# Kernel tuning notes

Hardware: AMD Instinct MI355X
Metric: run time of the kernel (lower is better)

The kernel has to match this reference:

```python
import jax, jax.numpy as jnp
import numpy as np

N_NODES = 50000
N_EDGES = 800000
FEAT = 128
HID1 = 128
HID2 = 64


def setup_inputs() -> dict:
    key = jax.random.key(0)
    k = jax.random.split(key, 6)
    x = jax.random.normal(k[0], (N_NODES, FEAT), dtype=jnp.float32)
    edge_index = jax.random.randint(k[1], (2, N_EDGES), 0, N_NODES, dtype=jnp.int32)
    # Glorot-style init scaling like PyG's GCNConv linear
    W1 = jax.random.normal(k[2], (FEAT, HID1), dtype=jnp.float32) * (1.0 / np.sqrt(FEAT))
    b1 = jnp.zeros((HID1,), dtype=jnp.float32)
    W2 = jax.random.normal(k[3], (HID1, HID2), dtype=jnp.float32) * (1.0 / np.sqrt(HID1))
    b2 = jnp.zeros((HID2,), dtype=jnp.float32)
    return {"x": x, "edge_index": edge_index, "W1": W1, "b1": b1, "W2": W2, "b2": b2}


def _gcn_conv(x, src, dst, W, b, n_nodes):
    """PyG GCNConv: h = X W; out_i = sum_j norm_ij h_j + b, with self-loops and
    symmetric normalization norm_ij = deg_i^-1/2 * deg_j^-1/2 (deg counts self-loop)."""
    h = x @ W  # [N, out]
    # degree at target nodes (self-loops already appended to src/dst)
    deg = jax.ops.segment_sum(jnp.ones_like(dst, dtype=h.dtype), dst, num_segments=n_nodes)
    dinv = jax.lax.rsqrt(jnp.maximum(deg, 1.0))  # deg >= 1 because of self-loops
    norm = dinv[src] * dinv[dst]  # [E+N]
    msg = h[src] * norm[:, None]  # gather + scale, [E+N, out]
    out = jax.ops.segment_sum(msg, dst, num_segments=n_nodes)
    return out + b


def reference(x, edge_index, W1, b1, W2, b2):
    n = x.shape[0]
    self_idx = jnp.arange(n, dtype=edge_index.dtype)
    src = jnp.concatenate([edge_index[0], self_idx])
    dst = jnp.concatenate([edge_index[1], self_idx])
    h = jax.nn.relu(_gcn_conv(x, src, dst, W1, b1, n))
    out = _gcn_conv(h, src, dst, W2, b2, n)
    return out
```

## Files before the change

kernel.cpp:

```cpp
#include <hip/hip_runtime.h>
#include <hip/hip_bf16.h>


#define POISON 0xAAAAAAAAu

typedef __attribute__((ext_vector_type(8))) short short8;
typedef __attribute__((ext_vector_type(4))) float f32x4;

__device__ __forceinline__ float bf_lo(unsigned u) { return __uint_as_float(u << 16); }
__device__ __forceinline__ float bf_hi(unsigned u) { return __uint_as_float(u & 0xffff0000u); }
__device__ __forceinline__ unsigned short f2bf(float f) {
    return (unsigned short)(__bfloat16_as_ushort(__float2bfloat16(f)));
}

__global__ __launch_bounds__(256) void countpack_kernel(
    const int* __restrict__ dst, unsigned* __restrict__ ucnt,
    unsigned short* __restrict__ eslot, int E,
    const float* __restrict__ W1, unsigned short* __restrict__ Wp1,
    const float* __restrict__ W2, unsigned short* __restrict__ Wp2) {
    constexpr int PB = (128 * 128 + 128 * 64) / 256;
    if ((int)blockIdx.x < PB) {
        int q = blockIdx.x * 256 + threadIdx.x;
        if (q < 128 * 128) {
            int j = q & 7;
            int n = (q >> 3) & 127;
            int kb = q >> 10;
            Wp1[q] = f2bf(W1[(kb * 8 + j) * 128 + n]);
        } else {
            int p = q - 128 * 128;
            int j = p & 7;
            int n = (p >> 3) & 63;
            int kb = p >> 9;
            Wp2[p] = f2bf(W2[(kb * 8 + j) * 64 + n]);
        }
        return;
    }
    int e0 = (blockIdx.x - PB) * 1024 + threadIdx.x * 4;
    if (e0 + 3 < E) {
        int4 d4 = *(const int4*)(dst + e0);
        ushort4 r;
        r.x = (unsigned short)(atomicAdd(&ucnt[d4.x], 1u) - POISON);
        r.y = (unsigned short)(atomicAdd(&ucnt[d4.y], 1u) - POISON);
        r.z = (unsigned short)(atomicAdd(&ucnt[d4.z], 1u) - POISON);
        r.w = (unsigned short)(atomicAdd(&ucnt[d4.w], 1u) - POISON);
        *(ushort4*)(eslot + e0) = r;
    } else {
        for (int e = e0; e < E; ++e)
            eslot[e] = (unsigned short)(atomicAdd(&ucnt[dst[e]], 1u) - POISON);
    }
}

__global__ __launch_bounds__(256) void alloc_kernel(unsigned* __restrict__ ucnt,
                                                    int* __restrict__ row_ptr,
                                                    float* __restrict__ dinv, int N) {
    int i = blockIdx.x * 256 + threadIdx.x;
    int lane = threadIdx.x & 63;
    int c = (i < N) ? (int)(ucnt[i] - POISON) : 0;
    if (i < N) dinv[i] = rsqrtf((float)(c + 1));
    int incl = c;
#pragma unroll
    for (int off = 1; off < 64; off <<= 1) {
        int u = __shfl_up(incl, off, 64);
        if (lane >= off) incl += u;
    }
    int base = 0;
    if (lane == 63) base = (int)(atomicAdd(&ucnt[N], (unsigned)incl) - POISON);
    base = __shfl(base, 63, 64);
    if (i < N) row_ptr[i] = base + incl - c;
}

__global__ __launch_bounds__(256) void scatgemm_kernel(
    const int* __restrict__ src, const int* __restrict__ dst,
    const int* __restrict__ row_ptr, const unsigned short* __restrict__ eslot,
    unsigned short* __restrict__ ssrc, int E,
    const float* __restrict__ X, const unsigned short* __restrict__ Wp1,
    const float* __restrict__ dinv, unsigned short* __restrict__ g1,
    int N, int gb) {
    if ((int)blockIdx.x >= gb) {
        int e0 = (blockIdx.x - gb) * 1024 + threadIdx.x * 4;
        if (e0 + 3 < E) {
            int4 d4 = *(const int4*)(dst + e0);
            int4 s4 = *(const int4*)(src + e0);
            ushort4 t4 = *(const ushort4*)(eslot + e0);
            ssrc[row_ptr[d4.x] + t4.x] = (unsigned short)s4.x;
            ssrc[row_ptr[d4.y] + t4.y] = (unsigned short)s4.y;
            ssrc[row_ptr[d4.z] + t4.z] = (unsigned short)s4.z;
            ssrc[row_ptr[d4.w] + t4.w] = (unsigned short)s4.w;
        } else {
            for (int e = e0; e < E; ++e)
                ssrc[row_ptr[dst[e]] + eslot[e]] = (unsigned short)src[e];
        }
        return;
    }
    constexpr int NT = 8;
    const int lane = threadIdx.x & 63;
    const int wave = threadIdx.x >> 6;
    const int col = lane & 15;
    const int quad = lane >> 4;
    const int row0w = (blockIdx.x * 4 + wave) * 16;

    int arow = row0w + col;
    if (arow >= N) arow = N - 1;

    short8 afr[4];
    const float* Xr = X + (size_t)arow * 128;
#pragma unroll
    for (int c = 0; c < 4; ++c) {
        float4 f0 = *(const float4*)(Xr + c * 32 + quad * 8);
        float4 f1 = *(const float4*)(Xr + c * 32 + quad * 8 + 4);
        short8 a;
        a[0] = (short)f2bf(f0.x); a[1] = (short)f2bf(f0.y);
        a[2] = (short)f2bf(f0.z); a[3] = (short)f2bf(f0.w);
        a[4] = (short)f2bf(f1.x); a[5] = (short)f2bf(f1.y);
        a[6] = (short)f2bf(f1.z); a[7] = (short)f2bf(f1.w);
        afr[c] = a;
    }

    f32x4 acc[NT];
#pragma unroll
    for (int t = 0; t < NT; ++t) acc[t] = (f32x4){0.f, 0.f, 0.f, 0.f};

    const uint4* Wq = (const uint4*)Wp1;
#pragma unroll
    for (int c = 0; c < 4; ++c) {
        short8 bfr[NT];
#pragma unroll
        for (int t = 0; t < NT; ++t) {
            union { uint4 u; short8 s; } cv;
            cv.u = Wq[(size_t)(c * 4 + quad) * 128 + t * 16 + col];
            bfr[t] = cv.s;
        }
#pragma unroll
        for (int t = 0; t < NT; ++t)
            acc[t] = __builtin_amdgcn_mfma_f32_16x16x32_bf16(afr[c], bfr[t], acc[t], 0, 0, 0);
    }

#pragma unroll
    for (int r = 0; r < 4; ++r) {
        int row = row0w + quad * 4 + r;
        if (row < N) {
            float dv = dinv[row];
#pragma unroll
            for (int t = 0; t < NT; ++t)
                g1[(size_t)row * 128 + t * 16 + col] = f2bf(acc[t][r] * dv);
        }
    }
}

#define AG1_BURST(NS)                                            \
    do {                                                         \
        unsigned v[NS];                                          \
        _Pragma("unroll") for (int t = 0; t < NS; ++t) {         \
            int s = __shfl(sidx, t, 64);                         \
            if (t >= rem) s = node;                              \
            v[t] = hp[(size_t)s * 64 + lane];                    \
        }                                                        \
        _Pragma("unroll") for (int t = 0; t < NS; ++t) {         \
            unsigned u = (t < rem) ? v[t] : 0u;                  \
            ax += bf_lo(u);                                      \
            ay += bf_hi(u);                                      \
        }                                                        \
    } while (0)

__global__ __launch_bounds__(256) void aggmm_kernel(const unsigned short* __restrict__ g1,
                                                    const int* __restrict__ row_ptr,
                                                    const unsigned* __restrict__ ucnt,
                                                    const unsigned short* __restrict__ ssrc,
                                                    const float* __restrict__ dinv,
                                                    const float* __restrict__ b1,
                                                    const unsigned short* __restrict__ Wp2,
                                                    unsigned short* __restrict__ g2, int N) {
    __shared__ unsigned short zt[16][136];
    __shared__ float sdinv[16];
    const int lane = threadIdx.x & 63;
    const int wave = threadIdx.x >> 6;
    const int nodebase = blockIdx.x * 16;
    const unsigned* hp = (const unsigned*)g1;

    const float bx = b1[2 * lane];
    const float by = b1[2 * lane + 1];

    for (int k = 0; k < 4; ++k) {
        int zr = wave * 4 + k;
        int node = __builtin_amdgcn_readfirstlane(nodebase + zr);
        unsigned pk = 0;
        if (node < N) {
            float di = dinv[node];
            int beg = row_ptr[node];
            int cnt = (int)(ucnt[node] - POISON);
            unsigned hv = hp[(size_t)node * 64 + lane];
            float ax = bf_lo(hv), ay = bf_hi(hv);
            for (int ch = 0; ch < cnt; ch += 24) {
                int rem = cnt - ch;
                int sidx = (int)ssrc[beg + ch + (lane & 31)];
                if (rem <= 8) AG1_BURST(8);
                else if (rem <= 16) AG1_BURST(16);
                else AG1_BURST(24);
            }
            float zx = fmaxf(ax * di + bx, 0.f);
            float zy = fmaxf(ay * di + by, 0.f);
            pk = (unsigned)f2bf(zx) | ((unsigned)f2bf(zy) << 16);
            if (lane == 0) sdinv[zr] = di;
        } else if (lane == 0) {
            sdinv[zr] = 0.f;
        }
        ((unsigned*)&zt[zr][0])[lane] = pk;
    }
    __syncthreads();

    const int col = lane & 15;
    const int quad = lane >> 4;
    short8 afr[4];
#pragma unroll
    for (int c = 0; c < 4; ++c) {
        union { uint4 u; short8 s; } cv;
        cv.u = *(const uint4*)&zt[col][c * 32 + quad * 8];
        afr[c] = cv.s;
    }
    f32x4 acc = (f32x4){0.f, 0.f, 0.f, 0.f};
    const uint4* Wq = (const uint4*)Wp2;
#pragma unroll
    for (int c = 0; c < 4; ++c) {
        union { uint4 u; short8 s; } cv;
        cv.u = Wq[(size_t)(c * 4 + quad) * 64 + wave * 16 + col];
        acc = __builtin_amdgcn_mfma_f32_16x16x32_bf16(afr[c], cv.s, acc, 0, 0, 0);
    }
#pragma unroll
    for (int r = 0; r < 4; ++r) {
        int row = nodebase + quad * 4 + r;
        if (row < N)
            g2[(size_t)row * 64 + wave * 16 + col] = f2bf(acc[r] * sdinv[quad * 4 + r]);
    }
}

#define AG2_BURST(NS)                                            \
    do {                                                         \
        unsigned v[NS];                                          \
        _Pragma("unroll") for (int t = 0; t < NS; ++t) {         \
            int s = __shfl(sidx, t, 64);                         \
            if (t >= rem) s = node;                              \
            v[t] = (unsigned)gp[(size_t)s * 64 + lane];          \
        }                                                        \
        _Pragma("unroll") for (int t = 0; t < NS; ++t) {         \
            unsigned u = (t < rem) ? v[t] : 0u;                  \
            ax += bf_lo(u);                                      \
        }                                                        \
    } while (0)

__global__ __launch_bounds__(256) void agg2_kernel(const unsigned short* __restrict__ gp,
                                                   const int* __restrict__ row_ptr,
                                                   const unsigned* __restrict__ ucnt,
                                                   const unsigned short* __restrict__ ssrc,
                                                   const float* __restrict__ dinv,
                                                   const float* __restrict__ bias,
                                                   float* __restrict__ out, int N) {
    int node = __builtin_amdgcn_readfirstlane((int)(blockIdx.x * 4 + (threadIdx.x >> 6)));
    if (node >= N) return;
    int lane = threadIdx.x & 63;
    float di = dinv[node];
    int beg = row_ptr[node];
    int cnt = (int)(ucnt[node] - POISON);

    float ax = bf_lo((unsigned)gp[(size_t)node * 64 + lane]);
    for (int ch = 0; ch < cnt; ch += 24) {
        int rem = cnt - ch;
        int sidx = (int)ssrc[beg + ch + (lane & 31)];
        if (rem <= 8) AG2_BURST(8);
        else if (rem <= 16) AG2_BURST(16);
        else AG2_BURST(24);
    }
    out[(size_t)node * 64 + lane] = ax * di + bias[lane];
}

extern "C" void kernel_launch(void* const* d_in, const int* in_sizes, int n_in,
                              void* d_out, int out_size, void* d_ws, size_t ws_size,
                              hipStream_t stream) {
    const float* x = (const float*)d_in[0];
    const int* eidx = (const int*)d_in[1];
    const float* W1 = (const float*)d_in[2];
    const float* b1 = (const float*)d_in[3];
    const float* W2 = (const float*)d_in[4];
    const float* b2 = (const float*)d_in[5];
    float* out = (float*)d_out;

    const int N = in_sizes[0] / 128;
    const int E = in_sizes[1] / 2;
    const int* src = eidx;
    const int* dst = eidx + E;

    char* ws = (char*)d_ws;
    size_t off = 0;
    auto alloc = [&](size_t bytes) -> char* {
        char* p = ws + off;
        off = (off + bytes + 255) & ~(size_t)255;
        return p;
    };
    unsigned* ucnt = (unsigned*)alloc((size_t)(N + 1) * 4);
    int* row_ptr = (int*)alloc((size_t)N * 4);
    unsigned short* eslot = (unsigned short*)alloc((size_t)(E + 16) * 2);
    unsigned short* ssrc = (unsigned short*)alloc((size_t)(E + 64) * 2);
    float* dinv = (float*)alloc((size_t)N * 4);
    unsigned short* Wp1 = (unsigned short*)alloc(128 * 128 * 2);
    unsigned short* Wp2 = (unsigned short*)alloc(128 * 64 * 2);
    unsigned short* g1 = (unsigned short*)alloc((size_t)N * 128 * 2);
    unsigned short* g2 = (unsigned short*)alloc((size_t)N * 64 * 2);
    (void)alloc(9 << 20);

    const int nbN = (N + 255) / 256;
    const int nbE4 = (E + 1023) / 1024;
    const int gb = (N + 63) / 64;
    constexpr int PB = (128 * 128 + 128 * 64) / 256;

    countpack_kernel<<<PB + nbE4, 256, 0, stream>>>(dst, ucnt, eslot, E, W1, Wp1, W2, Wp2);
    alloc_kernel<<<nbN, 256, 0, stream>>>(ucnt, row_ptr, dinv, N);
    scatgemm_kernel<<<gb + nbE4, 256, 0, stream>>>(src, dst, row_ptr, eslot, ssrc, E,
                                                   x, Wp1, dinv, g1, N, gb);
    aggmm_kernel<<<(N + 15) / 16, 256, 0, stream>>>(g1, row_ptr, ucnt, ssrc, dinv, b1, Wp2, g2, N);
    agg2_kernel<<<(N + 3) / 4, 256, 0, stream>>>(g2, row_ptr, ucnt, ssrc, dinv, b2, out, N);
}
```

Measured before the change: 192.9 us.

## Fuse five GCN kernels into one cooperative persistent kernel with grid syncs

Replaces the chain of five kernel launches (count/pack, allocate, scatter+GEMM, aggregate+GEMM, aggregate) with a single cooperative persistent kernel. The stages run in grid-stride loops separated by grid.sync(). The goal is to remove launch overhead and the inter-kernel drain gaps. In exchange, occupancy is capped at the cooperative grid size and each stage runs with fewer blocks. Grid-wide barriers add their own cost, and the original kernels remain as a fallback if the cooperative launch fails.

```diff
diff --git a/kernel.cpp b/kernel.cpp
--- a/kernel.cpp
+++ b/kernel.cpp
@@ -1,5 +1,8 @@
 #include <hip/hip_runtime.h>
 #include <hip/hip_bf16.h>
+#include <hip/hip_cooperative_groups.h>
+
+namespace cg = cooperative_groups;
 
 
 #define POISON 0xAAAAAAAAu
@@ -11,6 +14,262 @@
 __device__ __forceinline__ float bf_hi(unsigned u) { return __uint_as_float(u & 0xffff0000u); }
 __device__ __forceinline__ unsigned short f2bf(float f) {
     return (unsigned short)(__bfloat16_as_ushort(__float2bfloat16(f)));
+}
+
+#define AG1_BURST(NS)                                            \
+    do {                                                         \
+        unsigned v[NS];                                          \
+        _Pragma("unroll") for (int t = 0; t < NS; ++t) {         \
+            int s = __shfl(sidx, t, 64);                         \
+            if (t >= rem) s = node;                              \
+            v[t] = hp[(size_t)s * 64 + lane];                    \
+        }                                                        \
+        _Pragma("unroll") for (int t = 0; t < NS; ++t) {         \
+            unsigned u = (t < rem) ? v[t] : 0u;                  \
+            ax += bf_lo(u);                                      \
+            ay += bf_hi(u);                                      \
+        }                                                        \
+    } while (0)
+
+#define AG2_BURST(NS)                                            \
+    do {                                                         \
+        unsigned v[NS];                                          \
+        _Pragma("unroll") for (int t = 0; t < NS; ++t) {         \
+            int s = __shfl(sidx, t, 64);                         \
+            if (t >= rem) s = node;                              \
+            v[t] = (unsigned)gp[(size_t)s * 64 + lane];          \
+        }                                                        \
+        _Pragma("unroll") for (int t = 0; t < NS; ++t) {         \
+            unsigned u = (t < rem) ? v[t] : 0u;                  \
+            ax += bf_lo(u);                                      \
+        }                                                        \
+    } while (0)
+
+struct GcnParams {
+    const int* src;
+    const int* dst;
+    unsigned* ucnt;
+    int* row_ptr;
+    unsigned short* eslot;
+    unsigned short* ssrc;
+    float* dinv;
+    const float* X;
+    const float* W1;
+    const float* b1;
+    const float* W2;
+    const float* b2;
+    unsigned short* Wp1;
+    unsigned short* Wp2;
+    unsigned short* g1;
+    unsigned short* g2;
+    float* out;
+    int N, E, gb, nbN, nbE4, ngrp16, ngrp4;
+};
+
+__global__ __launch_bounds__(256, 6) void gcn_mega(GcnParams p) {
+    cg::grid_group grid = cg::this_grid();
+    const int tid = threadIdx.x;
+    const int lane = tid & 63;
+    const int wave = tid >> 6;
+    const int nblk = (int)gridDim.x;
+
+    __shared__ unsigned short zt[16][136];
+    __shared__ float sdinv[16];
+
+    for (int q = blockIdx.x * 256 + tid; q < 128 * 128 + 128 * 64; q += nblk * 256) {
+        if (q < 128 * 128) {
+            int j = q & 7;
+            int n = (q >> 3) & 127;
+            int kb = q >> 10;
+            p.Wp1[q] = f2bf(p.W1[(kb * 8 + j) * 128 + n]);
+        } else {
+            int r = q - 128 * 128;
+            int j = r & 7;
+            int n = (r >> 3) & 63;
+            int kb = r >> 9;
+            p.Wp2[r] = f2bf(p.W2[(kb * 8 + j) * 64 + n]);
+        }
+    }
+    for (int c = blockIdx.x; c < p.nbE4; c += nblk) {
+        int e0 = c * 1024 + tid * 4;
+        if (e0 + 3 < p.E) {
+            int4 d4 = *(const int4*)(p.dst + e0);
+            ushort4 r;
+            r.x = (unsigned short)(atomicAdd(&p.ucnt[d4.x], 1u) - POISON);
+            r.y = (unsigned short)(atomicAdd(&p.ucnt[d4.y], 1u) - POISON);
+            r.z = (unsigned short)(atomicAdd(&p.ucnt[d4.z], 1u) - POISON);
+            r.w = (unsigned short)(atomicAdd(&p.ucnt[d4.w], 1u) - POISON);
+            *(ushort4*)(p.eslot + e0) = r;
+        } else {
+            for (int e = e0; e < p.E; ++e)
+                p.eslot[e] = (unsigned short)(atomicAdd(&p.ucnt[p.dst[e]], 1u) - POISON);
+        }
+    }
+    grid.sync();
+
+    for (int bi = blockIdx.x; bi < p.nbN; bi += nblk) {
+        int i = bi * 256 + tid;
+        int c = (i < p.N) ? (int)(p.ucnt[i] - POISON) : 0;
+        if (i < p.N) p.dinv[i] = rsqrtf((float)(c + 1));
+        int incl = c;
+#pragma unroll
+        for (int off = 1; off < 64; off <<= 1) {
+            int u = __shfl_up(incl, off, 64);
+            if (lane >= off) incl += u;
+        }
+        int base = 0;
+        if (lane == 63) base = (int)(atomicAdd(&p.ucnt[p.N], (unsigned)incl) - POISON);
+        base = __shfl(base, 63, 64);
+        if (i < p.N) p.row_ptr[i] = base + incl - c;
+    }
+    grid.sync();
+
+    {
+        const int col = lane & 15;
+        const int quad = lane >> 4;
+        const uint4* Wq = (const uint4*)p.Wp1;
+        for (int t = blockIdx.x; t < p.gb; t += nblk) {
+            const int row0w = (t * 4 + wave) * 16;
+            int arow = row0w + col;
+            if (arow >= p.N) arow = p.N - 1;
+
+            short8 afr[4];
+            const float* Xr = p.X + (size_t)arow * 128;
+#pragma unroll
+            for (int cc = 0; cc < 4; ++cc) {
+                float4 f0 = *(const float4*)(Xr + cc * 32 + quad * 8);
+                float4 f1 = *(const float4*)(Xr + cc * 32 + quad * 8 + 4);
+                short8 a;
+                a[0] = (short)f2bf(f0.x); a[1] = (short)f2bf(f0.y);
+                a[2] = (short)f2bf(f0.z); a[3] = (short)f2bf(f0.w);
+                a[4] = (short)f2bf(f1.x); a[5] = (short)f2bf(f1.y);
+                a[6] = (short)f2bf(f1.z); a[7] = (short)f2bf(f1.w);
+                afr[cc] = a;
+            }
+            f32x4 acc[8];
+#pragma unroll
+            for (int tt = 0; tt < 8; ++tt) acc[tt] = (f32x4){0.f, 0.f, 0.f, 0.f};
+#pragma unroll
+            for (int cc = 0; cc < 4; ++cc) {
+#pragma unroll
+                for (int tt = 0; tt < 8; ++tt) {
+                    union { uint4 u; short8 s; } cv;
+                    cv.u = Wq[(size_t)(cc * 4 + quad) * 128 + tt * 16 + col];
+                    acc[tt] = __builtin_amdgcn_mfma_f32_16x16x32_bf16(afr[cc], cv.s, acc[tt], 0, 0, 0);
+                }
+            }
+#pragma unroll
+            for (int r = 0; r < 4; ++r) {
+                int row = row0w + quad * 4 + r;
+                if (row < p.N) {
+                    float dv = p.dinv[row];
+#pragma unroll
+                    for (int tt = 0; tt < 8; ++tt)
+                        p.g1[(size_t)row * 128 + tt * 16 + col] = f2bf(acc[tt][r] * dv);
+                }
+            }
+        }
+    }
+    for (int c = blockIdx.x; c < p.nbE4; c += nblk) {
+        int e0 = c * 1024 + tid * 4;
+        if (e0 + 3 < p.E) {
+            int4 d4 = *(const int4*)(p.dst + e0);
+            int4 s4 = *(const int4*)(p.src + e0);
+            ushort4 t4 = *(const ushort4*)(p.eslot + e0);
+            p.ssrc[p.row_ptr[d4.x] + t4.x] = (unsigned short)s4.x;
+            p.ssrc[p.row_ptr[d4.y] + t4.y] = (unsigned short)s4.y;
+            p.ssrc[p.row_ptr[d4.z] + t4.z] = (unsigned short)s4.z;
+            p.ssrc[p.row_ptr[d4.w] + t4.w] = (unsigned short)s4.w;
+        } else {
+            for (int e = e0; e < p.E; ++e)
+                p.ssrc[p.row_ptr[p.dst[e]] + p.eslot[e]] = (unsigned short)p.src[e];
+        }
+    }
+    grid.sync();
+
+    {
+        const unsigned* hp = (const unsigned*)p.g1;
+        const float bx = p.b1[2 * lane];
+        const float by = p.b1[2 * lane + 1];
+        const int col = lane & 15;
+        const int quad = lane >> 4;
+        const uint4* Wq = (const uint4*)p.Wp2;
+
+        for (int gr = blockIdx.x; gr < p.ngrp16; gr += nblk) {
+            const int nodebase = gr * 16;
+            for (int k = 0; k < 4; ++k) {
+                int zr = wave * 4 + k;
+                int node = __builtin_amdgcn_readfirstlane(nodebase + zr);
+                unsigned pk = 0;
+                if (node < p.N) {
+                    float di = p.dinv[node];
+                    int beg = p.row_ptr[node];
+                    int cnt = (int)(p.ucnt[node] - POISON);
+                    unsigned hv = hp[(size_t)node * 64 + lane];
+                    float ax = bf_lo(hv), ay = bf_hi(hv);
+                    for (int ch = 0; ch < cnt; ch += 24) {
+                        int rem = cnt - ch;
+                        int sidx = (int)p.ssrc[beg + ch + (lane & 31)];
+                        if (rem <= 8) AG1_BURST(8);
+                        else if (rem <= 16) AG1_BURST(16);
+                        else AG1_BURST(24);
+                    }
+                    float zx = fmaxf(ax * di + bx, 0.f);
+                    float zy = fmaxf(ay * di + by, 0.f);
+                    pk = (unsigned)f2bf(zx) | ((unsigned)f2bf(zy) << 16);
+                    if (lane == 0) sdinv[zr] = di;
+                } else if (lane == 0) {
+                    sdinv[zr] = 0.f;
+                }
+                ((unsigned*)&zt[zr][0])[lane] = pk;
+            }
+            __syncthreads();
+            short8 afr[4];
+#pragma unroll
+            for (int cc = 0; cc < 4; ++cc) {
+                union { uint4 u; short8 s; } cv;
+                cv.u = *(const uint4*)&zt[col][cc * 32 + quad * 8];
+                afr[cc] = cv.s;
+            }
+            f32x4 acc = (f32x4){0.f, 0.f, 0.f, 0.f};
+#pragma unroll
+            for (int cc = 0; cc < 4; ++cc) {
+                union { uint4 u; short8 s; } cv;
+                cv.u = Wq[(size_t)(cc * 4 + quad) * 64 + wave * 16 + col];
+                acc = __builtin_amdgcn_mfma_f32_16x16x32_bf16(afr[cc], cv.s, acc, 0, 0, 0);
+            }
+#pragma unroll
+            for (int r = 0; r < 4; ++r) {
+                int row = nodebase + quad * 4 + r;
+                if (row < p.N)
+                    p.g2[(size_t)row * 64 + wave * 16 + col] =
+                        f2bf(acc[r] * sdinv[quad * 4 + r]);
+            }
+            __syncthreads();
+        }
+    }
+    grid.sync();
+
+    {
+        const unsigned short* gp = p.g2;
+        const float bv = p.b2[lane];
+        for (int gr = blockIdx.x; gr < p.ngrp4; gr += nblk) {
+            int node = __builtin_amdgcn_readfirstlane(gr * 4 + wave);
+            if (node >= p.N) continue;
+            float di = p.dinv[node];
+            int beg = p.row_ptr[node];
+            int cnt = (int)(p.ucnt[node] - POISON);
+            float ax = bf_lo((unsigned)gp[(size_t)node * 64 + lane]);
+            for (int ch = 0; ch < cnt; ch += 24) {
+                int rem = cnt - ch;
+                int sidx = (int)p.ssrc[beg + ch + (lane & 31)];
+                if (rem <= 8) AG2_BURST(8);
+                else if (rem <= 16) AG2_BURST(16);
+                else AG2_BURST(24);
+            }
+            p.out[(size_t)node * 64 + lane] = ax * di + bv;
+        }
+    }
 }
 
 __global__ __launch_bounds__(256) void countpack_kernel(
@@ -27,11 +286,11 @@
             int kb = q >> 10;
             Wp1[q] = f2bf(W1[(kb * 8 + j) * 128 + n]);
         } else {
-            int p = q - 128 * 128;
-            int j = p & 7;
-            int n = (p >> 3) & 63;
-            int kb = p >> 9;
-            Wp2[p] = f2bf(W2[(kb * 8 + j) * 64 + n]);
+            int r = q - 128 * 128;
+            int j = r & 7;
+            int n = (r >> 3) & 63;
+            int kb = r >> 9;
+            Wp2[r] = f2bf(W2[(kb * 8 + j) * 64 + n]);
         }
         return;
     }
@@ -115,11 +374,9 @@
         a[6] = (short)f2bf(f1.z); a[7] = (short)f2bf(f1.w);
         afr[c] = a;
     }
-
     f32x4 acc[NT];
 #pragma unroll
     for (int t = 0; t < NT; ++t) acc[t] = (f32x4){0.f, 0.f, 0.f, 0.f};
-
     const uint4* Wq = (const uint4*)Wp1;
 #pragma unroll
     for (int c = 0; c < 4; ++c) {
@@ -134,7 +391,6 @@
         for (int t = 0; t < NT; ++t)
             acc[t] = __builtin_amdgcn_mfma_f32_16x16x32_bf16(afr[c], bfr[t], acc[t], 0, 0, 0);
     }
-
 #pragma unroll
     for (int r = 0; r < 4; ++r) {
         int row = row0w + quad * 4 + r;
@@ -146,21 +402,6 @@
         }
     }
 }
-
-#define AG1_BURST(NS)                                            \
-    do {                                                         \
-        unsigned v[NS];                                          \
-        _Pragma("unroll") for (int t = 0; t < NS; ++t) {         \
-            int s = __shfl(sidx, t, 64);                         \
-            if (t >= rem) s = node;                              \
-            v[t] = hp[(size_t)s * 64 + lane];                    \
-        }                                                        \
-        _Pragma("unroll") for (int t = 0; t < NS; ++t) {         \
-            unsigned u = (t < rem) ? v[t] : 0u;                  \
-            ax += bf_lo(u);                                      \
-            ay += bf_hi(u);                                      \
-        }                                                        \
-    } while (0)
 
 __global__ __launch_bounds__(256) void aggmm_kernel(const unsigned short* __restrict__ g1,
                                                     const int* __restrict__ row_ptr,
@@ -232,20 +473,6 @@
             g2[(size_t)row * 64 + wave * 16 + col] = f2bf(acc[r] * sdinv[quad * 4 + r]);
     }
 }
-
-#define AG2_BURST(NS)                                            \
-    do {                                                         \
-        unsigned v[NS];                                          \
-        _Pragma("unroll") for (int t = 0; t < NS; ++t) {         \
-            int s = __shfl(sidx, t, 64);                         \
-            if (t >= rem) s = node;                              \
-            v[t] = (unsigned)gp[(size_t)s * 64 + lane];          \
-        }                                                        \
-        _Pragma("unroll") for (int t = 0; t < NS; ++t) {         \
-            unsigned u = (t < rem) ? v[t] : 0u;                  \
-            ax += bf_lo(u);                                      \
-        }                                                        \
-    } while (0)
 
 __global__ __launch_bounds__(256) void agg2_kernel(const unsigned short* __restrict__ gp,
                                                    const int* __restrict__ row_ptr,
@@ -311,10 +538,52 @@
     const int gb = (N + 63) / 64;
     constexpr int PB = (128 * 128 + 128 * 64) / 256;
 
-    countpack_kernel<<<PB + nbE4, 256, 0, stream>>>(dst, ucnt, eslot, E, W1, Wp1, W2, Wp2);
-    alloc_kernel<<<nbN, 256, 0, stream>>>(ucnt, row_ptr, dinv, N);
-    scatgemm_kernel<<<gb + nbE4, 256, 0, stream>>>(src, dst, row_ptr, eslot, ssrc, E,
-                                                   x, Wp1, dinv, g1, N, gb);
-    aggmm_kernel<<<(N + 15) / 16, 256, 0, stream>>>(g1, row_ptr, ucnt, ssrc, dinv, b1, Wp2, g2, N);
-    agg2_kernel<<<(N + 3) / 4, 256, 0, stream>>>(g2, row_ptr, ucnt, ssrc, dinv, b2, out, N);
-}
+    GcnParams P;
+    P.src = src; P.dst = dst;
+    P.ucnt = ucnt; P.row_ptr = row_ptr; P.eslot = eslot; P.ssrc = ssrc;
+    P.dinv = dinv;
+    P.X = x; P.W1 = W1; P.b1 = b1; P.W2 = W2; P.b2 = b2;
+    P.Wp1 = Wp1; P.Wp2 = Wp2; P.g1 = g1; P.g2 = g2; P.out = out;
+    P.N = N; P.E = E; P.gb = gb; P.nbN = nbN; P.nbE4 = nbE4;
+    P.ngrp16 = (N + 15) / 16;
+    P.ngrp4 = (N + 3) / 4;
+
+    static int coopGrid = -1;
+    if (coopGrid < 0) {
+        int maxbPerCU = 0;
+        hipError_t qe = hipOccupancyMaxActiveBlocksPerMultiprocessor(&maxbPerCU, gcn_mega, 256, 0);
+        int numCU = 0;
+        hipError_t ae = hipDeviceGetAttribute(&numCU, hipDeviceAttributeMultiprocessorCount, 0);
+        if (qe == hipSuccess && ae == hipSuccess && maxbPerCU > 0 && numCU > 0) {
+            long g = (long)maxbPerCU * numCU;
+            if (g > 2048) g = 2048;
+            coopGrid = (int)g;
+        } else {
+            coopGrid = 0;
+        }
+    }
+
+    bool launched = false;
+    if (coopGrid > 0) {
+        void* kargs[] = {(void*)&P};
+        hipError_t err = hipLaunchCooperativeKernel((const void*)gcn_mega, dim3(coopGrid),
+                                                    dim3(256), kargs, 0, stream);
+        if (err == hipSuccess) {
+            launched = true;
+        } else {
+            (void)hipGetLastError();
+            coopGrid = 0;
+        }
+    }
+
+    if (!launched) {
+        const int nbE4b = nbE4;
+        countpack_kernel<<<PB + nbE4b, 256, 0, stream>>>(dst, ucnt, eslot, E, W1, Wp1, W2, Wp2);
+        alloc_kernel<<<nbN, 256, 0, stream>>>(ucnt, row_ptr, dinv, N);
+        scatgemm_kernel<<<gb + nbE4b, 256, 0, stream>>>(src, dst, row_ptr, eslot, ssrc, E,
+                                                        x, Wp1, dinv, g1, N, gb);
+        aggmm_kernel<<<(N + 15) / 16, 256, 0, stream>>>(g1, row_ptr, ucnt, ssrc, dinv, b1,
+                                                        Wp2, g2, N);
+        agg2_kernel<<<(N + 3) / 4, 256, 0, stream>>>(g2, row_ptr, ucnt, ssrc, dinv, b2, out, N);
+    }
+}
```

After: 618.5 us. +220.6%, slower.
